# Kernel tuning notes

Measured on AMD Instinct MI355X. Metric: run time of the kernel, lower is better.

Reference implementation:

```python
import jax, jax.numpy as jnp
import numpy as np

N = 2048            # num nodes
AVG_DEG = 16
E0 = N * AVG_DEG    # random edges; self-loops appended -> E = E0 + N
IN_FEATS = 256
H = 16              # num_heads
HS = 32             # hidden_size (forced by linear001 = Linear(32,16))
D = HS // H         # head_dim = 2
EPS = 1e-5


def gat_conv(x, src, dst, W, al, ar, b):
    # DGL-style GATConv: x [N,F] -> [N,H,D]
    feat = (x @ W).reshape(N, H, D)                      # [N,H,D]
    el = (feat * al[None]).sum(-1)                       # [N,H] (src term)
    er = (feat * ar[None]).sum(-1)                       # [N,H] (dst term)
    e = jax.nn.leaky_relu(el[src] + er[dst], 0.2)        # [E,H]
    m = jax.ops.segment_max(e, dst, num_segments=N)      # segment softmax over incoming edges
    ex = jnp.exp(e - m[dst])
    s = jax.ops.segment_sum(ex, dst, num_segments=N)
    alpha = ex / s[dst]                                  # [E,H]
    out = jax.ops.segment_sum(alpha[:, :, None] * feat[src], dst, num_segments=N)
    return out + b.reshape(1, H, D)


def setup_inputs() -> dict:
    key = jax.random.key(0)
    ks = jax.random.split(key, 40)
    rn = lambda k, s, sc=0.1: (jax.random.normal(k, s, jnp.float32) * sc)
    loops = jnp.arange(N, dtype=jnp.int32)
    src = jnp.concatenate([jax.random.randint(ks[0], (E0,), 0, N, jnp.int32), loops])
    dst = jnp.concatenate([jax.random.randint(ks[1], (E0,), 0, N, jnp.int32), loops])
    inp = {
        'features': jax.random.normal(ks[2], (N, IN_FEATS), jnp.float32),
        'src': src, 'dst': dst,
        # GATConv 1
        'W1': rn(ks[3], (IN_FEATS, HS)), 'al1': rn(ks[4], (H, D)), 'ar1': rn(ks[5], (H, D)), 'bg1': rn(ks[6], (HS,)),
        # GATConv 2
        'W2': rn(ks[7], (HS, HS)), 'al2': rn(ks[8], (H, D)), 'ar2': rn(ks[9], (H, D)), 'bg2': rn(ks[10], (HS,)),
        # dense MHA projections
        'qw': rn(ks[11], (HS, HS)), 'qb': rn(ks[12], (HS,)),
        'kw': rn(ks[13], (HS, HS)), 'kb': rn(ks[14], (HS,)),
        'vw': rn(ks[15], (HS, HS)), 'vb': rn(ks[16], (HS,)),
        'ow': rn(ks[17], (HS, HS)), 'ob': rn(ks[18], (HS,)),
        # batchnorm affine
        'bn_g': jnp.ones((HS,), jnp.float32), 'bn_b': jnp.zeros((HS,), jnp.float32),
        # mlp
        'm1w': rn(ks[19], (HS, HS // 2)), 'm1b': rn(ks[20], (HS // 2,)),
        'm2w': rn(ks[21], (HS // 2, HS)), 'm2b': rn(ks[22], (HS,)),
        # scoring head
        'w001': rn(ks[23], (32, 16)), 'b001': rn(ks[24], (16,)),
        'w01': rn(ks[25], (16, 8)), 'b01': rn(ks[26], (8,)),
        'w1': rn(ks[27], (8, 4)), 'b1': rn(ks[28], (4,)),
        'w2': rn(ks[29], (4, 1)), 'b2': rn(ks[30], (1,)),
    }
    return inp


def reference(features, src, dst, W1, al1, ar1, bg1, W2, al2, ar2, bg2,
              qw, qb, kw, kb, vw, vb, ow, ob, bn_g, bn_b,
              m1w, m1b, m2w, m2b, w001, b001, w01, b01, w1, b1, w2, b2):
    h = gat_conv(features, src, dst, W1, al1, ar1, bg1).reshape(N, HS)
    h = gat_conv(h, src, dst, W2, al2, ar2, bg2).reshape(N, HS)
    # manual dense multi-head attention across all nodes
    Q = (h @ qw + qb).reshape(N, H, D)
    K = (h @ kw + kb).reshape(N, H, D)
    V = (h @ vw + vb).reshape(N, H, D)
    scores = jnp.einsum('nhd,mhd->hnm', Q, K) / jnp.sqrt(jnp.float32(D))  # [H,N,N]
    attn = jax.nn.softmax(scores, axis=-1)
    ao = jnp.einsum('hnm,mhd->nhd', attn, V).reshape(N, HS)
    ao = ao @ ow + ob
    # BatchNorm1d (training mode: batch stats, biased variance)
    mu = ao.mean(0)
    var = ao.var(0)
    ao = (ao - mu) / jnp.sqrt(var + EPS) * bn_g + bn_b
    # MLP
    ao = jax.nn.relu(ao @ m1w + m1b)
    ao = jax.nn.relu(ao @ m2w + m2b)
    # scoring head
    z = jax.nn.leaky_relu(ao @ w001 + b001, 0.01)
    z = jax.nn.leaky_relu(z @ w01 + b01, 0.01)
    z = jax.nn.leaky_relu(z @ w1 + b1, 0.01)
    return jax.nn.sigmoid(z @ w2 + b2)  # [N,1]
```

## Files before the change

kernel.cpp:

```cpp
#include <hip/hip_runtime.h>
#include <math.h>

#define NN 2048
#define NH 16
#define HSZ 32
#define INF_ 256

__global__ void k_gat1(const float* __restrict__ x, const float* __restrict__ W,
                       const float* __restrict__ al, const float* __restrict__ ar,
                       float* __restrict__ feat, float* __restrict__ el,
                       float* __restrict__ er, int* __restrict__ cnt,
                       int* __restrict__ cur, float* __restrict__ bnbuf) {
    __shared__ float xs[INF_];
    __shared__ float ps[256];
    __shared__ float fs[HSZ];
    int n = blockIdx.x, tid = threadIdx.x;
    xs[tid] = x[(size_t)n * INF_ + tid];
    if (tid == 0) cnt[n] = 0;
    if (tid == 1) cur[n] = 0;
    if (n == 0 && tid >= 128 && tid < 192) bnbuf[tid - 128] = 0.f;
    __syncthreads();
    int j = tid & 31, part = tid >> 5;
    float a = 0.f;
#pragma unroll
    for (int kk = 0; kk < 32; ++kk) {
        int k = part * 32 + kk;
        a += xs[k] * W[k * HSZ + j];
    }
    ps[tid] = a;
    __syncthreads();
    if (tid < HSZ) {
        float s = 0.f;
#pragma unroll
        for (int p = 0; p < 8; ++p) s += ps[p * 32 + tid];
        fs[tid] = s;
        feat[n * HSZ + tid] = s;
    }
    __syncthreads();
    if (tid < NH) {
        el[n * NH + tid] = fs[2 * tid] * al[2 * tid] + fs[2 * tid + 1] * al[2 * tid + 1];
    } else if (tid < 2 * NH) {
        int hh = tid - NH;
        er[n * NH + hh] = fs[2 * hh] * ar[2 * hh] + fs[2 * hh + 1] * ar[2 * hh + 1];
    }
}

__global__ void k_hist(int E, const int* __restrict__ dst, int* __restrict__ cnt) {
    int i = blockIdx.x * 256 + threadIdx.x;
    if (i < E) atomicAdd(&cnt[dst[i]], 1);
}

__global__ void k_scan(const int* __restrict__ cnt, int* __restrict__ off, int E) {
    __shared__ int ps[256];
    int t = threadIdx.x;
    int base = t * 8;
    int loc[8];
    int s = 0;
#pragma unroll
    for (int j = 0; j < 8; ++j) {
        loc[j] = s;
        s += cnt[base + j];
    }
    ps[t] = s;
    __syncthreads();
    for (int st = 1; st < 256; st <<= 1) {
        int v = (t >= st) ? ps[t - st] : 0;
        __syncthreads();
        ps[t] += v;
        __syncthreads();
    }
    int chunkbase = ps[t] - s;
#pragma unroll
    for (int j = 0; j < 8; ++j) off[base + j] = chunkbase + loc[j];
    if (t == 255) off[NN] = chunkbase + s;
}

__global__ void k_scatter(int E, const int* __restrict__ src, const int* __restrict__ dst,
                          const int* __restrict__ off, int* __restrict__ cur,
                          int* __restrict__ adj) {
    int i = blockIdx.x * 256 + threadIdx.x;
    if (i >= E) return;
    int d = dst[i];
    int p = atomicAdd(&cur[d], 1);
    adj[off[d] + p] = src[i];
}

__global__ void k_seg(const int* __restrict__ off, const int* __restrict__ adj,
                      const float* __restrict__ el, const float* __restrict__ er,
                      const float* __restrict__ feat, const float* __restrict__ bias,
                      float* __restrict__ hout) {
    int i = blockIdx.x * 256 + threadIdx.x;
    int n = i >> 4, h = i & 15;
    int o0 = off[n], o1 = off[n + 1];
    float erv = er[n * NH + h];
    float sum = 0.f, a0 = 0.f, a1 = 0.f;
    for (int j = o0; j < o1; ++j) {
        int s = adj[j];
        float v = el[s * NH + h] + erv;
        v = v > 0.f ? v : 0.2f * v;
        float ex = __expf(v);
        float2 f = ((const float2*)feat)[s * NH + h];
        sum += ex;
        a0 += ex * f.x;
        a1 += ex * f.y;
    }
    float rs = 1.f / sum;
    hout[n * HSZ + 2 * h] = a0 * rs + bias[2 * h];
    hout[n * HSZ + 2 * h + 1] = a1 * rs + bias[2 * h + 1];
}

__global__ void k_gat2(const float* __restrict__ h1, const float* __restrict__ W,
                       const float* __restrict__ al, const float* __restrict__ ar,
                       float* __restrict__ feat, float* __restrict__ el,
                       float* __restrict__ er) {
    __shared__ float hs[256];
    __shared__ float fs[256];
    int tid = threadIdx.x;
    int row0 = blockIdx.x * 8;
    int r = tid >> 5, j = tid & 31;
    hs[tid] = h1[row0 * HSZ + tid];
    __syncthreads();
    float a = 0.f;
#pragma unroll
    for (int c = 0; c < HSZ; ++c) a += hs[r * HSZ + c] * W[c * HSZ + j];
    fs[tid] = a;
    feat[row0 * HSZ + tid] = a;
    __syncthreads();
    if (tid < 128) {
        int rr = tid >> 4, hh = tid & 15;
        el[(row0 + rr) * NH + hh] =
            fs[rr * HSZ + 2 * hh] * al[2 * hh] + fs[rr * HSZ + 2 * hh + 1] * al[2 * hh + 1];
    } else {
        int t = tid - 128;
        int rr = t >> 4, hh = t & 15;
        er[(row0 + rr) * NH + hh] =
            fs[rr * HSZ + 2 * hh] * ar[2 * hh] + fs[rr * HSZ + 2 * hh + 1] * ar[2 * hh + 1];
    }
}

__global__ void k_qkv(const float* __restrict__ h2, const float* __restrict__ qw,
                      const float* __restrict__ qb, const float* __restrict__ kw,
                      const float* __restrict__ kb, const float* __restrict__ vw,
                      const float* __restrict__ vb, float* __restrict__ Q,
                      float* __restrict__ Kt, float* __restrict__ Vt) {
    __shared__ float hs[256];
    int tid = threadIdx.x;
    int row0 = blockIdx.x * 8;
    int r = tid >> 5, j = tid & 31;
    int n = row0 + r;
    hs[tid] = h2[row0 * HSZ + tid];
    __syncthreads();
    float q = qb[j], k = kb[j], v = vb[j];
#pragma unroll
    for (int c = 0; c < HSZ; ++c) {
        float hv = hs[r * HSZ + c];
        q += hv * qw[c * HSZ + j];
        k += hv * kw[c * HSZ + j];
        v += hv * vw[c * HSZ + j];
    }
    Q[n * HSZ + j] = q * 0.70710678118654752f;
    int hh = j >> 1, d = j & 1;
    Kt[hh * (NN * 2) + n * 2 + d] = k;
    Vt[hh * (NN * 2) + n * 2 + d] = v;
}

__global__ void k_attn(const float* __restrict__ Q, const float* __restrict__ Kt,
                       const float* __restrict__ Vt, float* __restrict__ ao) {
    int gtid = blockIdx.x * 256 + threadIdx.x;
    int wid = gtid >> 6;
    int lane = gtid & 63;
    int hh = wid >> 8;
    int q0 = (wid & 255) * 8;
    const float2* K2 = (const float2*)Kt + hh * NN;
    const float2* V2 = (const float2*)Vt + hh * NN;
    float qx[8], qy[8];
#pragma unroll
    for (int i = 0; i < 8; ++i) {
        float2 qq = ((const float2*)Q)[(q0 + i) * NH + hh];
        qx[i] = qq.x;
        qy[i] = qq.y;
    }
    float sm[8], a0[8], a1[8];
#pragma unroll
    for (int i = 0; i < 8; ++i) { sm[i] = 0.f; a0[i] = 0.f; a1[i] = 0.f; }
#pragma unroll 2
    for (int it = 0; it < NN / 64; ++it) {
        int mm = it * 64 + lane;
        float2 kk = K2[mm];
        float2 vv = V2[mm];
#pragma unroll
        for (int i = 0; i < 8; ++i) {
            float p = __expf(qx[i] * kk.x + qy[i] * kk.y);
            sm[i] += p;
            a0[i] += p * vv.x;
            a1[i] += p * vv.y;
        }
    }
#pragma unroll
    for (int i = 0; i < 8; ++i) {
#pragma unroll
        for (int off = 32; off > 0; off >>= 1) {
            sm[i] += __shfl_xor(sm[i], off);
            a0[i] += __shfl_xor(a0[i], off);
            a1[i] += __shfl_xor(a1[i], off);
        }
        if (lane == 0) {
            float rs = 1.f / sm[i];
            ((float2*)ao)[(q0 + i) * NH + hh] = make_float2(a0[i] * rs, a1[i] * rs);
        }
    }
}

__global__ void k_oproj(const float* __restrict__ ao, const float* __restrict__ ow,
                        const float* __restrict__ ob, float* __restrict__ X,
                        float* __restrict__ bnbuf) {
    __shared__ float as[256];
    __shared__ float xv[256];
    int tid = threadIdx.x;
    int row0 = blockIdx.x * 8;
    as[tid] = ao[row0 * HSZ + tid];
    __syncthreads();
    int r = tid >> 5, j = tid & 31;
    float a = ob[j];
#pragma unroll
    for (int c = 0; c < HSZ; ++c) a += as[r * HSZ + c] * ow[c * HSZ + j];
    X[(row0 + r) * HSZ + j] = a;
    xv[tid] = a;
    __syncthreads();
    if (tid < HSZ) {
        float s = 0.f, q = 0.f;
#pragma unroll
        for (int rr = 0; rr < 8; ++rr) {
            float v = xv[rr * HSZ + tid];
            s += v;
            q += v * v;
        }
        atomicAdd(&bnbuf[tid], s);
        atomicAdd(&bnbuf[HSZ + tid], q);
    }
}

__global__ void k_tail(const float* __restrict__ X, const float* __restrict__ bnbuf,
                       const float* __restrict__ bn_g, const float* __restrict__ bn_b,
                       const float* __restrict__ m1w, const float* __restrict__ m1b,
                       const float* __restrict__ m2w, const float* __restrict__ m2b,
                       const float* __restrict__ w001, const float* __restrict__ b001,
                       const float* __restrict__ w01, const float* __restrict__ b01,
                       const float* __restrict__ w1, const float* __restrict__ b1,
                       const float* __restrict__ w2, const float* __restrict__ b2,
                       float* __restrict__ out) {
    int n = blockIdx.x * 256 + threadIdx.x;
    const float invN = 1.f / NN;
    float x[HSZ];
#pragma unroll
    for (int i = 0; i < HSZ; ++i) {
        float mu = bnbuf[i] * invN;
        float var = bnbuf[HSZ + i] * invN - mu * mu;
        float rstd = rsqrtf(var + 1e-5f);
        x[i] = (X[n * HSZ + i] - mu) * rstd * bn_g[i] + bn_b[i];
    }
    float y[16];
#pragma unroll
    for (int j = 0; j < 16; ++j) {
        float a = m1b[j];
#pragma unroll
        for (int i = 0; i < HSZ; ++i) a += x[i] * m1w[i * 16 + j];
        y[j] = fmaxf(a, 0.f);
    }
    float z[HSZ];
#pragma unroll
    for (int j = 0; j < HSZ; ++j) {
        float a = m2b[j];
#pragma unroll
        for (int i = 0; i < 16; ++i) a += y[i] * m2w[i * HSZ + j];
        z[j] = fmaxf(a, 0.f);
    }
    float a16[16];
#pragma unroll
    for (int j = 0; j < 16; ++j) {
        float a = b001[j];
#pragma unroll
        for (int i = 0; i < HSZ; ++i) a += z[i] * w001[i * 16 + j];
        a16[j] = a > 0.f ? a : 0.01f * a;
    }
    float b8[8];
#pragma unroll
    for (int j = 0; j < 8; ++j) {
        float a = b01[j];
#pragma unroll
        for (int i = 0; i < 16; ++i) a += a16[i] * w01[i * 8 + j];
        b8[j] = a > 0.f ? a : 0.01f * a;
    }
    float c4[4];
#pragma unroll
    for (int j = 0; j < 4; ++j) {
        float a = b1[j];
#pragma unroll
        for (int i = 0; i < 8; ++i) a += b8[i] * w1[i * 4 + j];
        c4[j] = a > 0.f ? a : 0.01f * a;
    }
    float d = b2[0];
#pragma unroll
    for (int i = 0; i < 4; ++i) d += c4[i] * w2[i];
    out[n] = 1.f / (1.f + __expf(-d));
}

extern "C" void kernel_launch(void* const* d_in, const int* in_sizes, int n_in,
                              void* d_out, int out_size, void* d_ws, size_t ws_size,
                              hipStream_t stream) {
    const float* features = (const float*)d_in[0];
    const int* src = (const int*)d_in[1];
    const int* dst = (const int*)d_in[2];
    const float* W1 = (const float*)d_in[3];
    const float* al1 = (const float*)d_in[4];
    const float* ar1 = (const float*)d_in[5];
    const float* bg1 = (const float*)d_in[6];
    const float* W2 = (const float*)d_in[7];
    const float* al2 = (const float*)d_in[8];
    const float* ar2 = (const float*)d_in[9];
    const float* bg2 = (const float*)d_in[10];
    const float* qw = (const float*)d_in[11];
    const float* qb = (const float*)d_in[12];
    const float* kw = (const float*)d_in[13];
    const float* kb = (const float*)d_in[14];
    const float* vw = (const float*)d_in[15];
    const float* vb = (const float*)d_in[16];
    const float* ow = (const float*)d_in[17];
    const float* ob = (const float*)d_in[18];
    const float* bn_g = (const float*)d_in[19];
    const float* bn_b = (const float*)d_in[20];
    const float* m1w = (const float*)d_in[21];
    const float* m1b = (const float*)d_in[22];
    const float* m2w = (const float*)d_in[23];
    const float* m2b = (const float*)d_in[24];
    const float* w001 = (const float*)d_in[25];
    const float* b001 = (const float*)d_in[26];
    const float* w01 = (const float*)d_in[27];
    const float* b01 = (const float*)d_in[28];
    const float* w1 = (const float*)d_in[29];
    const float* b1 = (const float*)d_in[30];
    const float* w2 = (const float*)d_in[31];
    const float* b2 = (const float*)d_in[32];

    int E = in_sizes[1];

    float* ws = (float*)d_ws;
    float* feat = ws;
    float* el = feat + NN * HSZ;
    float* er = el + NN * NH;
    float* h1 = er + NN * NH;
    float* h2 = h1 + NN * HSZ;
    float* Q = h2 + NN * HSZ;
    float* Kt = Q + NN * HSZ;
    float* Vt = Kt + NN * HSZ;
    float* ao = Vt + NN * HSZ;
    float* X = ao + NN * HSZ;
    float* bnbuf = X + NN * HSZ;
    int* cnt = (int*)(bnbuf + 64);
    int* cur = cnt + NN;
    int* off = cur + NN;
    int* adj = off + NN + 1;

    dim3 b256(256);
    int gE = (E + 255) / 256;

    k_gat1<<<NN, b256, 0, stream>>>(features, W1, al1, ar1, feat, el, er, cnt, cur, bnbuf);
    k_hist<<<gE, b256, 0, stream>>>(E, dst, cnt);
    k_scan<<<1, b256, 0, stream>>>(cnt, off, E);
    k_scatter<<<gE, b256, 0, stream>>>(E, src, dst, off, cur, adj);
    k_seg<<<(NN * NH) / 256, b256, 0, stream>>>(off, adj, el, er, feat, bg1, h1);
    k_gat2<<<NN / 8, b256, 0, stream>>>(h1, W2, al2, ar2, feat, el, er);
    k_seg<<<(NN * NH) / 256, b256, 0, stream>>>(off, adj, el, er, feat, bg2, h2);
    k_qkv<<<NN / 8, b256, 0, stream>>>(h2, qw, qb, kw, kb, vw, vb, Q, Kt, Vt);
    k_attn<<<(NN * NH) / (8 * 4), b256, 0, stream>>>(Q, Kt, Vt, ao);
    k_oproj<<<NN / 8, b256, 0, stream>>>(ao, ow, ob, X, bnbuf);
    k_tail<<<NN / 256, b256, 0, stream>>>(X, bnbuf, bn_g, bn_b, m1w, m1b, m2w, m2b,
                                          w001, b001, w01, b01, w1, b1, w2, b2,
                                          (float*)d_out);
}
```

Baseline: 217.6 us.

## Fuse whole pipeline into persistent megakernel with grid barriers and atomic edge aggregation

Replaces the eleven separate kernel launches with a single persistent kernel of 256 blocks that moves between phases through software grid barriers built on agent-scope atomics. The CSR build (histogram, scan, scatter) is dropped. Each edge phase now does per-edge atomicAdd accumulation of the softmax numerator and denominator into per-destination buffers. Attention, output projection and batchnorm statistics are fused per block, and the MLP tail runs after the last barrier. This aims to remove launch overhead and the adjacency build, but it adds heavy atomic contention, lowers parallelism in the attention phase (1024 waves instead of 4096), and relies on a barrier-reset protocol that could race across repeated launches.

```diff
diff --git a/kernel.cpp b/kernel.cpp
--- a/kernel.cpp
+++ b/kernel.cpp
@@ -5,376 +5,362 @@
 #define NH 16
 #define HSZ 32
 #define INF_ 256
-
-__global__ void k_gat1(const float* __restrict__ x, const float* __restrict__ W,
-                       const float* __restrict__ al, const float* __restrict__ ar,
-                       float* __restrict__ feat, float* __restrict__ el,
-                       float* __restrict__ er, int* __restrict__ cnt,
-                       int* __restrict__ cur, float* __restrict__ bnbuf) {
-    __shared__ float xs[INF_];
-    __shared__ float ps[256];
-    __shared__ float fs[HSZ];
-    int n = blockIdx.x, tid = threadIdx.x;
-    xs[tid] = x[(size_t)n * INF_ + tid];
-    if (tid == 0) cnt[n] = 0;
-    if (tid == 1) cur[n] = 0;
-    if (n == 0 && tid >= 128 && tid < 192) bnbuf[tid - 128] = 0.f;
-    __syncthreads();
-    int j = tid & 31, part = tid >> 5;
-    float a = 0.f;
-#pragma unroll
-    for (int kk = 0; kk < 32; ++kk) {
-        int k = part * 32 + kk;
-        a += xs[k] * W[k * HSZ + j];
-    }
-    ps[tid] = a;
-    __syncthreads();
-    if (tid < HSZ) {
-        float s = 0.f;
-#pragma unroll
-        for (int p = 0; p < 8; ++p) s += ps[p * 32 + tid];
-        fs[tid] = s;
-        feat[n * HSZ + tid] = s;
-    }
-    __syncthreads();
-    if (tid < NH) {
-        el[n * NH + tid] = fs[2 * tid] * al[2 * tid] + fs[2 * tid + 1] * al[2 * tid + 1];
-    } else if (tid < 2 * NH) {
-        int hh = tid - NH;
-        er[n * NH + hh] = fs[2 * hh] * ar[2 * hh] + fs[2 * hh + 1] * ar[2 * hh + 1];
-    }
-}
-
-__global__ void k_hist(int E, const int* __restrict__ dst, int* __restrict__ cnt) {
-    int i = blockIdx.x * 256 + threadIdx.x;
-    if (i < E) atomicAdd(&cnt[dst[i]], 1);
-}
-
-__global__ void k_scan(const int* __restrict__ cnt, int* __restrict__ off, int E) {
-    __shared__ int ps[256];
-    int t = threadIdx.x;
-    int base = t * 8;
-    int loc[8];
-    int s = 0;
-#pragma unroll
-    for (int j = 0; j < 8; ++j) {
-        loc[j] = s;
-        s += cnt[base + j];
-    }
-    ps[t] = s;
-    __syncthreads();
-    for (int st = 1; st < 256; st <<= 1) {
-        int v = (t >= st) ? ps[t - st] : 0;
-        __syncthreads();
-        ps[t] += v;
-        __syncthreads();
-    }
-    int chunkbase = ps[t] - s;
-#pragma unroll
-    for (int j = 0; j < 8; ++j) off[base + j] = chunkbase + loc[j];
-    if (t == 255) off[NN] = chunkbase + s;
-}
-
-__global__ void k_scatter(int E, const int* __restrict__ src, const int* __restrict__ dst,
-                          const int* __restrict__ off, int* __restrict__ cur,
-                          int* __restrict__ adj) {
-    int i = blockIdx.x * 256 + threadIdx.x;
-    if (i >= E) return;
-    int d = dst[i];
-    int p = atomicAdd(&cur[d], 1);
-    adj[off[d] + p] = src[i];
-}
-
-__global__ void k_seg(const int* __restrict__ off, const int* __restrict__ adj,
-                      const float* __restrict__ el, const float* __restrict__ er,
-                      const float* __restrict__ feat, const float* __restrict__ bias,
-                      float* __restrict__ hout) {
-    int i = blockIdx.x * 256 + threadIdx.x;
-    int n = i >> 4, h = i & 15;
-    int o0 = off[n], o1 = off[n + 1];
-    float erv = er[n * NH + h];
-    float sum = 0.f, a0 = 0.f, a1 = 0.f;
-    for (int j = o0; j < o1; ++j) {
-        int s = adj[j];
-        float v = el[s * NH + h] + erv;
+#define NBLK 256
+#define NTHR 256
+#define NTOT (NBLK * NTHR)
+#define DOOR_MAGIC 0x1357bd1
+
+struct Params {
+    const float *x, *W1, *al1, *ar1, *bg1, *W2, *al2, *ar2, *bg2;
+    const float *qw, *qb, *kw, *kb, *vw, *vb, *ow, *ob;
+    const float *bn_g, *bn_b, *m1w, *m1b, *m2w, *m2b;
+    const float *w001, *b001, *w01, *b01, *w1v, *b1v, *w2v, *b2v;
+    const int *src, *dst;
+    float *feat, *el, *er, *ssumA, *accA, *ssumB, *accB, *bnbuf;
+    float *Q, *Kt, *Vt, *X, *out;
+    int *bar;
+    int E;
+};
+
+__device__ __forceinline__ void gbar(int* __restrict__ bar, int slot, bool first) {
+    __threadfence();
+    __syncthreads();
+    if (threadIdx.x == 0) {
+        if (first) {
+            while (__hip_atomic_load(&bar[7], __ATOMIC_ACQUIRE,
+                                     __HIP_MEMORY_SCOPE_AGENT) != DOOR_MAGIC)
+                __builtin_amdgcn_s_sleep(2);
+        }
+        __hip_atomic_fetch_add(&bar[slot], 1, __ATOMIC_ACQ_REL,
+                               __HIP_MEMORY_SCOPE_AGENT);
+        while (__hip_atomic_load(&bar[slot], __ATOMIC_ACQUIRE,
+                                 __HIP_MEMORY_SCOPE_AGENT) < NBLK)
+            __builtin_amdgcn_s_sleep(2);
+    }
+    __syncthreads();
+    __threadfence();
+}
+
+__device__ __forceinline__ void edge_phase(const int* __restrict__ src,
+                                           const int* __restrict__ dst,
+                                           const float* __restrict__ el,
+                                           const float* __restrict__ er,
+                                           const float* __restrict__ feat,
+                                           float* __restrict__ ssum,
+                                           float* __restrict__ acc, int E, int gtid) {
+    int EH = E * NH;
+    for (int i = gtid; i < EH; i += NTOT) {
+        int e = i >> 4, h = i & 15;
+        int s = src[e], d = dst[e];
+        float v = el[s * NH + h] + er[d * NH + h];
         v = v > 0.f ? v : 0.2f * v;
         float ex = __expf(v);
         float2 f = ((const float2*)feat)[s * NH + h];
-        sum += ex;
-        a0 += ex * f.x;
-        a1 += ex * f.y;
-    }
-    float rs = 1.f / sum;
-    hout[n * HSZ + 2 * h] = a0 * rs + bias[2 * h];
-    hout[n * HSZ + 2 * h + 1] = a1 * rs + bias[2 * h + 1];
-}
-
-__global__ void k_gat2(const float* __restrict__ h1, const float* __restrict__ W,
-                       const float* __restrict__ al, const float* __restrict__ ar,
-                       float* __restrict__ feat, float* __restrict__ el,
-                       float* __restrict__ er) {
-    __shared__ float hs[256];
-    __shared__ float fs[256];
-    int tid = threadIdx.x;
-    int row0 = blockIdx.x * 8;
+        atomicAdd(&ssum[d * NH + h], ex);
+        atomicAdd(&acc[(d * NH + h) * 2 + 0], ex * f.x);
+        atomicAdd(&acc[(d * NH + h) * 2 + 1], ex * f.y);
+    }
+}
+
+__device__ __forceinline__ void gat_phase(const float* __restrict__ acc,
+                                          const float* __restrict__ ssum,
+                                          const float* __restrict__ bias,
+                                          const float* __restrict__ W,
+                                          const float* __restrict__ al,
+                                          const float* __restrict__ ar,
+                                          float* __restrict__ feat, float* __restrict__ el,
+                                          float* __restrict__ er, float* shA, float* shB,
+                                          int blk, int tid) {
     int r = tid >> 5, j = tid & 31;
-    hs[tid] = h1[row0 * HSZ + tid];
+    int row0 = blk * 8;
+    int n = row0 + r;
+    shA[tid] = acc[n * HSZ + j] / ssum[n * NH + (j >> 1)] + bias[j];
     __syncthreads();
     float a = 0.f;
 #pragma unroll
-    for (int c = 0; c < HSZ; ++c) a += hs[r * HSZ + c] * W[c * HSZ + j];
-    fs[tid] = a;
+    for (int c = 0; c < HSZ; ++c) a += shA[r * HSZ + c] * W[c * HSZ + j];
+    shB[tid] = a;
     feat[row0 * HSZ + tid] = a;
     __syncthreads();
     if (tid < 128) {
         int rr = tid >> 4, hh = tid & 15;
         el[(row0 + rr) * NH + hh] =
-            fs[rr * HSZ + 2 * hh] * al[2 * hh] + fs[rr * HSZ + 2 * hh + 1] * al[2 * hh + 1];
+            shB[rr * HSZ + 2 * hh] * al[2 * hh] + shB[rr * HSZ + 2 * hh + 1] * al[2 * hh + 1];
     } else {
-        int t = tid - 128;
-        int rr = t >> 4, hh = t & 15;
+        int t = tid - 128, rr = t >> 4, hh = t & 15;
         er[(row0 + rr) * NH + hh] =
-            fs[rr * HSZ + 2 * hh] * ar[2 * hh] + fs[rr * HSZ + 2 * hh + 1] * ar[2 * hh + 1];
-    }
-}
-
-__global__ void k_qkv(const float* __restrict__ h2, const float* __restrict__ qw,
-                      const float* __restrict__ qb, const float* __restrict__ kw,
-                      const float* __restrict__ kb, const float* __restrict__ vw,
-                      const float* __restrict__ vb, float* __restrict__ Q,
-                      float* __restrict__ Kt, float* __restrict__ Vt) {
-    __shared__ float hs[256];
-    int tid = threadIdx.x;
-    int row0 = blockIdx.x * 8;
-    int r = tid >> 5, j = tid & 31;
-    int n = row0 + r;
-    hs[tid] = h2[row0 * HSZ + tid];
-    __syncthreads();
-    float q = qb[j], k = kb[j], v = vb[j];
-#pragma unroll
-    for (int c = 0; c < HSZ; ++c) {
-        float hv = hs[r * HSZ + c];
-        q += hv * qw[c * HSZ + j];
-        k += hv * kw[c * HSZ + j];
-        v += hv * vw[c * HSZ + j];
-    }
-    Q[n * HSZ + j] = q * 0.70710678118654752f;
-    int hh = j >> 1, d = j & 1;
-    Kt[hh * (NN * 2) + n * 2 + d] = k;
-    Vt[hh * (NN * 2) + n * 2 + d] = v;
-}
-
-__global__ void k_attn(const float* __restrict__ Q, const float* __restrict__ Kt,
-                       const float* __restrict__ Vt, float* __restrict__ ao) {
-    int gtid = blockIdx.x * 256 + threadIdx.x;
-    int wid = gtid >> 6;
-    int lane = gtid & 63;
-    int hh = wid >> 8;
-    int q0 = (wid & 255) * 8;
-    const float2* K2 = (const float2*)Kt + hh * NN;
-    const float2* V2 = (const float2*)Vt + hh * NN;
-    float qx[8], qy[8];
-#pragma unroll
-    for (int i = 0; i < 8; ++i) {
-        float2 qq = ((const float2*)Q)[(q0 + i) * NH + hh];
-        qx[i] = qq.x;
-        qy[i] = qq.y;
-    }
-    float sm[8], a0[8], a1[8];
-#pragma unroll
-    for (int i = 0; i < 8; ++i) { sm[i] = 0.f; a0[i] = 0.f; a1[i] = 0.f; }
+            shB[rr * HSZ + 2 * hh] * ar[2 * hh] + shB[rr * HSZ + 2 * hh + 1] * ar[2 * hh + 1];
+    }
+    __syncthreads();
+}
+
+__global__ void __launch_bounds__(NTHR, 1) mega(Params p) {
+    __shared__ float shA[256];
+    __shared__ float shB[256];
+    const int tid = threadIdx.x;
+    const int blk = blockIdx.x;
+    const int gtid = blk * NTHR + tid;
+
+    if (blk == 0) {
+        if (tid < 7)
+            __hip_atomic_store(&p.bar[tid], 0, __ATOMIC_RELAXED,
+                               __HIP_MEMORY_SCOPE_AGENT);
+        __threadfence();
+        __syncthreads();
+        if (tid == 0)
+            __hip_atomic_store(&p.bar[7], DOOR_MAGIC, __ATOMIC_RELEASE,
+                               __HIP_MEMORY_SCOPE_AGENT);
+    }
+
+    {
+        float* z = p.ssumA;
+        const int ztot = NN * 96 + 64;
+        for (int i = gtid; i < ztot; i += NTOT) z[i] = 0.f;
+    }
+    {
+        int j = tid & 31, part = tid >> 5;
+        for (int r = 0; r < 8; ++r) {
+            int n = blk * 8 + r;
+            shA[tid] = p.x[(size_t)n * INF_ + tid];
+            __syncthreads();
+            float a = 0.f;
+#pragma unroll
+            for (int kk = 0; kk < 32; ++kk) {
+                int k = part * 32 + kk;
+                a += shA[k] * p.W1[k * HSZ + j];
+            }
+            shB[tid] = a;
+            __syncthreads();
+            if (tid < HSZ) {
+                float s = 0.f;
+#pragma unroll
+                for (int q = 0; q < 8; ++q) s += shB[q * 32 + tid];
+                p.feat[n * HSZ + tid] = s;
+                shA[tid] = s;
+            }
+            __syncthreads();
+            if (tid < NH) {
+                p.el[n * NH + tid] =
+                    shA[2 * tid] * p.al1[2 * tid] + shA[2 * tid + 1] * p.al1[2 * tid + 1];
+            } else if (tid < 2 * NH) {
+                int hh = tid - NH;
+                p.er[n * NH + hh] =
+                    shA[2 * hh] * p.ar1[2 * hh] + shA[2 * hh + 1] * p.ar1[2 * hh + 1];
+            }
+            __syncthreads();
+        }
+    }
+    gbar(p.bar, 0, true);
+
+    edge_phase(p.src, p.dst, p.el, p.er, p.feat, p.ssumA, p.accA, p.E, gtid);
+    gbar(p.bar, 1, false);
+
+    gat_phase(p.accA, p.ssumA, p.bg1, p.W2, p.al2, p.ar2, p.feat, p.el, p.er, shA, shB,
+              blk, tid);
+    gbar(p.bar, 2, false);
+
+    edge_phase(p.src, p.dst, p.el, p.er, p.feat, p.ssumB, p.accB, p.E, gtid);
+    gbar(p.bar, 3, false);
+
+    {
+        int r = tid >> 5, j = tid & 31;
+        int row0 = blk * 8;
+        int n = row0 + r;
+        shA[tid] = p.accB[n * HSZ + j] / p.ssumB[n * NH + (j >> 1)] + p.bg2[j];
+        __syncthreads();
+        float q = p.qb[j], k = p.kb[j], v = p.vb[j];
+#pragma unroll
+        for (int c = 0; c < HSZ; ++c) {
+            float hv = shA[r * HSZ + c];
+            q += hv * p.qw[c * HSZ + j];
+            k += hv * p.kw[c * HSZ + j];
+            v += hv * p.vw[c * HSZ + j];
+        }
+        p.Q[n * HSZ + j] = q * 0.70710678118654752f;
+        int hh = j >> 1, d2 = j & 1;
+        p.Kt[hh * (NN * 2) + n * 2 + d2] = k;
+        p.Vt[hh * (NN * 2) + n * 2 + d2] = v;
+        __syncthreads();
+    }
+    gbar(p.bar, 4, false);
+
+    {
+        int wave = tid >> 6, lane = tid & 63;
+        int row0 = blk * 8;
+        for (int h = wave; h < NH; h += 4) {
+            float qx[8], qy[8];
+#pragma unroll
+            for (int i = 0; i < 8; ++i) {
+                float2 qq = ((const float2*)p.Q)[(row0 + i) * NH + h];
+                qx[i] = qq.x;
+                qy[i] = qq.y;
+            }
+            const float2* K2 = (const float2*)p.Kt + h * NN;
+            const float2* V2 = (const float2*)p.Vt + h * NN;
+            float sm[8], a0[8], a1[8];
+#pragma unroll
+            for (int i = 0; i < 8; ++i) { sm[i] = 0.f; a0[i] = 0.f; a1[i] = 0.f; }
 #pragma unroll 2
-    for (int it = 0; it < NN / 64; ++it) {
-        int mm = it * 64 + lane;
-        float2 kk = K2[mm];
-        float2 vv = V2[mm];
-#pragma unroll
-        for (int i = 0; i < 8; ++i) {
-            float p = __expf(qx[i] * kk.x + qy[i] * kk.y);
-            sm[i] += p;
-            a0[i] += p * vv.x;
-            a1[i] += p * vv.y;
-        }
-    }
-#pragma unroll
-    for (int i = 0; i < 8; ++i) {
-#pragma unroll
-        for (int off = 32; off > 0; off >>= 1) {
-            sm[i] += __shfl_xor(sm[i], off);
-            a0[i] += __shfl_xor(a0[i], off);
-            a1[i] += __shfl_xor(a1[i], off);
-        }
-        if (lane == 0) {
-            float rs = 1.f / sm[i];
-            ((float2*)ao)[(q0 + i) * NH + hh] = make_float2(a0[i] * rs, a1[i] * rs);
-        }
-    }
-}
-
-__global__ void k_oproj(const float* __restrict__ ao, const float* __restrict__ ow,
-                        const float* __restrict__ ob, float* __restrict__ X,
-                        float* __restrict__ bnbuf) {
-    __shared__ float as[256];
-    __shared__ float xv[256];
-    int tid = threadIdx.x;
-    int row0 = blockIdx.x * 8;
-    as[tid] = ao[row0 * HSZ + tid];
-    __syncthreads();
-    int r = tid >> 5, j = tid & 31;
-    float a = ob[j];
-#pragma unroll
-    for (int c = 0; c < HSZ; ++c) a += as[r * HSZ + c] * ow[c * HSZ + j];
-    X[(row0 + r) * HSZ + j] = a;
-    xv[tid] = a;
-    __syncthreads();
-    if (tid < HSZ) {
-        float s = 0.f, q = 0.f;
-#pragma unroll
-        for (int rr = 0; rr < 8; ++rr) {
-            float v = xv[rr * HSZ + tid];
-            s += v;
-            q += v * v;
-        }
-        atomicAdd(&bnbuf[tid], s);
-        atomicAdd(&bnbuf[HSZ + tid], q);
-    }
-}
-
-__global__ void k_tail(const float* __restrict__ X, const float* __restrict__ bnbuf,
-                       const float* __restrict__ bn_g, const float* __restrict__ bn_b,
-                       const float* __restrict__ m1w, const float* __restrict__ m1b,
-                       const float* __restrict__ m2w, const float* __restrict__ m2b,
-                       const float* __restrict__ w001, const float* __restrict__ b001,
-                       const float* __restrict__ w01, const float* __restrict__ b01,
-                       const float* __restrict__ w1, const float* __restrict__ b1,
-                       const float* __restrict__ w2, const float* __restrict__ b2,
-                       float* __restrict__ out) {
-    int n = blockIdx.x * 256 + threadIdx.x;
-    const float invN = 1.f / NN;
-    float x[HSZ];
-#pragma unroll
-    for (int i = 0; i < HSZ; ++i) {
-        float mu = bnbuf[i] * invN;
-        float var = bnbuf[HSZ + i] * invN - mu * mu;
-        float rstd = rsqrtf(var + 1e-5f);
-        x[i] = (X[n * HSZ + i] - mu) * rstd * bn_g[i] + bn_b[i];
-    }
-    float y[16];
-#pragma unroll
-    for (int j = 0; j < 16; ++j) {
-        float a = m1b[j];
-#pragma unroll
-        for (int i = 0; i < HSZ; ++i) a += x[i] * m1w[i * 16 + j];
-        y[j] = fmaxf(a, 0.f);
-    }
-    float z[HSZ];
-#pragma unroll
-    for (int j = 0; j < HSZ; ++j) {
-        float a = m2b[j];
-#pragma unroll
-        for (int i = 0; i < 16; ++i) a += y[i] * m2w[i * HSZ + j];
-        z[j] = fmaxf(a, 0.f);
-    }
-    float a16[16];
-#pragma unroll
-    for (int j = 0; j < 16; ++j) {
-        float a = b001[j];
-#pragma unroll
-        for (int i = 0; i < HSZ; ++i) a += z[i] * w001[i * 16 + j];
-        a16[j] = a > 0.f ? a : 0.01f * a;
-    }
-    float b8[8];
-#pragma unroll
-    for (int j = 0; j < 8; ++j) {
-        float a = b01[j];
-#pragma unroll
-        for (int i = 0; i < 16; ++i) a += a16[i] * w01[i * 8 + j];
-        b8[j] = a > 0.f ? a : 0.01f * a;
-    }
-    float c4[4];
-#pragma unroll
-    for (int j = 0; j < 4; ++j) {
-        float a = b1[j];
-#pragma unroll
-        for (int i = 0; i < 8; ++i) a += b8[i] * w1[i * 4 + j];
-        c4[j] = a > 0.f ? a : 0.01f * a;
-    }
-    float d = b2[0];
-#pragma unroll
-    for (int i = 0; i < 4; ++i) d += c4[i] * w2[i];
-    out[n] = 1.f / (1.f + __expf(-d));
+            for (int it = 0; it < NN / 64; ++it) {
+                float2 kk = K2[it * 64 + lane];
+                float2 vv = V2[it * 64 + lane];
+#pragma unroll
+                for (int i = 0; i < 8; ++i) {
+                    float pp = __expf(qx[i] * kk.x + qy[i] * kk.y);
+                    sm[i] += pp;
+                    a0[i] += pp * vv.x;
+                    a1[i] += pp * vv.y;
+                }
+            }
+#pragma unroll
+            for (int i = 0; i < 8; ++i) {
+#pragma unroll
+                for (int off = 32; off > 0; off >>= 1) {
+                    sm[i] += __shfl_xor(sm[i], off);
+                    a0[i] += __shfl_xor(a0[i], off);
+                    a1[i] += __shfl_xor(a1[i], off);
+                }
+                if (lane == 0) {
+                    float rs = 1.f / sm[i];
+                    shA[i * HSZ + 2 * h] = a0[i] * rs;
+                    shA[i * HSZ + 2 * h + 1] = a1[i] * rs;
+                }
+            }
+        }
+        __syncthreads();
+        int r = tid >> 5, j = tid & 31;
+        float a = p.ob[j];
+#pragma unroll
+        for (int c = 0; c < HSZ; ++c) a += shA[r * HSZ + c] * p.ow[c * HSZ + j];
+        p.X[(row0 + r) * HSZ + j] = a;
+        shB[tid] = a;
+        __syncthreads();
+        if (tid < HSZ) {
+            float s = 0.f, q = 0.f;
+#pragma unroll
+            for (int rr = 0; rr < 8; ++rr) {
+                float v = shB[rr * HSZ + tid];
+                s += v;
+                q += v * v;
+            }
+            atomicAdd(&p.bnbuf[tid], s);
+            atomicAdd(&p.bnbuf[HSZ + tid], q);
+        }
+    }
+    gbar(p.bar, 5, false);
+
+    if (gtid < NN) {
+        int n = gtid;
+        const float invN = 1.f / NN;
+        float xr[HSZ];
+#pragma unroll
+        for (int i = 0; i < HSZ; ++i) {
+            float mu = p.bnbuf[i] * invN;
+            float var = p.bnbuf[HSZ + i] * invN - mu * mu;
+            float rstd = rsqrtf(var + 1e-5f);
+            xr[i] = (p.X[n * HSZ + i] - mu) * rstd * p.bn_g[i] + p.bn_b[i];
+        }
+        float y[16];
+#pragma unroll
+        for (int j = 0; j < 16; ++j) {
+            float a = p.m1b[j];
+#pragma unroll
+            for (int i = 0; i < HSZ; ++i) a += xr[i] * p.m1w[i * 16 + j];
+            y[j] = fmaxf(a, 0.f);
+        }
+        float z[HSZ];
+#pragma unroll
+        for (int j = 0; j < HSZ; ++j) {
+            float a = p.m2b[j];
+#pragma unroll
+            for (int i = 0; i < 16; ++i) a += y[i] * p.m2w[i * HSZ + j];
+            z[j] = fmaxf(a, 0.f);
+        }
+        float a16[16];
+#pragma unroll
+        for (int j = 0; j < 16; ++j) {
+            float a = p.b001[j];
+#pragma unroll
+            for (int i = 0; i < HSZ; ++i) a += z[i] * p.w001[i * 16 + j];
+            a16[j] = a > 0.f ? a : 0.01f * a;
+        }
+        float b8[8];
+#pragma unroll
+        for (int j = 0; j < 8; ++j) {
+            float a = p.b01[j];
+#pragma unroll
+            for (int i = 0; i < 16; ++i) a += a16[i] * p.w01[i * 8 + j];
+            b8[j] = a > 0.f ? a : 0.01f * a;
+        }
+        float c4[4];
+#pragma unroll
+        for (int j = 0; j < 4; ++j) {
+            float a = p.b1v[j];
+#pragma unroll
+            for (int i = 0; i < 8; ++i) a += b8[i] * p.w1v[i * 4 + j];
+            c4[j] = a > 0.f ? a : 0.01f * a;
+        }
+        float d = p.b2v[0];
+#pragma unroll
+        for (int i = 0; i < 4; ++i) d += c4[i] * p.w2v[i];
+        p.out[n] = 1.f / (1.f + __expf(-d));
+    }
 }
 
 extern "C" void kernel_launch(void* const* d_in, const int* in_sizes, int n_in,
                               void* d_out, int out_size, void* d_ws, size_t ws_size,
                               hipStream_t stream) {
-    const float* features = (const float*)d_in[0];
-    const int* src = (const int*)d_in[1];
-    const int* dst = (const int*)d_in[2];
-    const float* W1 = (const float*)d_in[3];
-    const float* al1 = (const float*)d_in[4];
-    const float* ar1 = (const float*)d_in[5];
-    const float* bg1 = (const float*)d_in[6];
-    const float* W2 = (const float*)d_in[7];
-    const float* al2 = (const float*)d_in[8];
-    const float* ar2 = (const float*)d_in[9];
-    const float* bg2 = (const float*)d_in[10];
-    const float* qw = (const float*)d_in[11];
-    const float* qb = (const float*)d_in[12];
-    const float* kw = (const float*)d_in[13];
-    const float* kb = (const float*)d_in[14];
-    const float* vw = (const float*)d_in[15];
-    const float* vb = (const float*)d_in[16];
-    const float* ow = (const float*)d_in[17];
-    const float* ob = (const float*)d_in[18];
-    const float* bn_g = (const float*)d_in[19];
-    const float* bn_b = (const float*)d_in[20];
-    const float* m1w = (const float*)d_in[21];
-    const float* m1b = (const float*)d_in[22];
-    const float* m2w = (const float*)d_in[23];
-    const float* m2b = (const float*)d_in[24];
-    const float* w001 = (const float*)d_in[25];
-    const float* b001 = (const float*)d_in[26];
-    const float* w01 = (const float*)d_in[27];
-    const float* b01 = (const float*)d_in[28];
-    const float* w1 = (const float*)d_in[29];
-    const float* b1 = (const float*)d_in[30];
-    const float* w2 = (const float*)d_in[31];
-    const float* b2 = (const float*)d_in[32];
-
-    int E = in_sizes[1];
+    Params p;
+    p.x = (const float*)d_in[0];
+    p.src = (const int*)d_in[1];
+    p.dst = (const int*)d_in[2];
+    p.W1 = (const float*)d_in[3];
+    p.al1 = (const float*)d_in[4];
+    p.ar1 = (const float*)d_in[5];
+    p.bg1 = (const float*)d_in[6];
+    p.W2 = (const float*)d_in[7];
+    p.al2 = (const float*)d_in[8];
+    p.ar2 = (const float*)d_in[9];
+    p.bg2 = (const float*)d_in[10];
+    p.qw = (const float*)d_in[11];
+    p.qb = (const float*)d_in[12];
+    p.kw = (const float*)d_in[13];
+    p.kb = (const float*)d_in[14];
+    p.vw = (const float*)d_in[15];
+    p.vb = (const float*)d_in[16];
+    p.ow = (const float*)d_in[17];
+    p.ob = (const float*)d_in[18];
+    p.bn_g = (const float*)d_in[19];
+    p.bn_b = (const float*)d_in[20];
+    p.m1w = (const float*)d_in[21];
+    p.m1b = (const float*)d_in[22];
+    p.m2w = (const float*)d_in[23];
+    p.m2b = (const float*)d_in[24];
+    p.w001 = (const float*)d_in[25];
+    p.b001 = (const float*)d_in[26];
+    p.w01 = (const float*)d_in[27];
+    p.b01 = (const float*)d_in[28];
+    p.w1v = (const float*)d_in[29];
+    p.b1v = (const float*)d_in[30];
+    p.w2v = (const float*)d_in[31];
+    p.b2v = (const float*)d_in[32];
+    p.E = in_sizes[1];
 
     float* ws = (float*)d_ws;
-    float* feat = ws;
-    float* el = feat + NN * HSZ;
-    float* er = el + NN * NH;
-    float* h1 = er + NN * NH;
-    float* h2 = h1 + NN * HSZ;
-    float* Q = h2 + NN * HSZ;
-    float* Kt = Q + NN * HSZ;
-    float* Vt = Kt + NN * HSZ;
-    float* ao = Vt + NN * HSZ;
-    float* X = ao + NN * HSZ;
-    float* bnbuf = X + NN * HSZ;
-    int* cnt = (int*)(bnbuf + 64);
-    int* cur = cnt + NN;
-    int* off = cur + NN;
-    int* adj = off + NN + 1;
-
-    dim3 b256(256);
-    int gE = (E + 255) / 256;
-
-    k_gat1<<<NN, b256, 0, stream>>>(features, W1, al1, ar1, feat, el, er, cnt, cur, bnbuf);
-    k_hist<<<gE, b256, 0, stream>>>(E, dst, cnt);
-    k_scan<<<1, b256, 0, stream>>>(cnt, off, E);
-    k_scatter<<<gE, b256, 0, stream>>>(E, src, dst, off, cur, adj);
-    k_seg<<<(NN * NH) / 256, b256, 0, stream>>>(off, adj, el, er, feat, bg1, h1);
-    k_gat2<<<NN / 8, b256, 0, stream>>>(h1, W2, al2, ar2, feat, el, er);
-    k_seg<<<(NN * NH) / 256, b256, 0, stream>>>(off, adj, el, er, feat, bg2, h2);
-    k_qkv<<<NN / 8, b256, 0, stream>>>(h2, qw, qb, kw, kb, vw, vb, Q, Kt, Vt);
-    k_attn<<<(NN * NH) / (8 * 4), b256, 0, stream>>>(Q, Kt, Vt, ao);
-    k_oproj<<<NN / 8, b256, 0, stream>>>(ao, ow, ob, X, bnbuf);
-    k_tail<<<NN / 256, b256, 0, stream>>>(X, bnbuf, bn_g, bn_b, m1w, m1b, m2w, m2b,
-                                          w001, b001, w01, b01, w1, b1, w2, b2,
-                                          (float*)d_out);
-}
+    p.feat = ws;
+    p.el = p.feat + NN * HSZ;
+    p.er = p.el + NN * NH;
+    p.ssumA = p.er + NN * NH;
+    p.accA = p.ssumA + NN * NH;
+    p.ssumB = p.accA + NN * HSZ;
+    p.accB = p.ssumB + NN * NH;
+    p.bnbuf = p.accB + NN * HSZ;
+    p.Q = p.bnbuf + 64;
+    p.Kt = p.Q + NN * HSZ;
+    p.Vt = p.Kt + NN * HSZ;
+    p.X = p.Vt + NN * HSZ;
+    p.bar = (int*)(p.X + NN * HSZ);
+    p.out = (float*)d_out;
+
+    mega<<<dim3(NBLK), dim3(NTHR), 0, stream>>>(p);
+}
```

Result: slower. 497.1 us (+128.5%).
